# Performance work log

Measured on AMD Instinct MI355X. Metric: run time of the kernel, lower is better.

Reference implementation:

```python
import jax, jax.numpy as jnp
import numpy as np

N_INTERVALS = 40          # control intervals (240 = 6 * n)
DT = 0.25                 # interval_duration
CAR_WIDTH = 2.0
N_OBST = 3                # (13 - 4) / 3
BATCH = 131072


def _dynamics(state, u, t):
    # state: (..., 4) = [px, py, theta, v]; u: (..., 2) = [accel, omega]
    px, py, th, v = state[..., 0], state[..., 1], state[..., 2], state[..., 3]
    a, w = u[..., 0], u[..., 1]
    return jnp.stack([px + v * jnp.cos(th) * t,
                      py + v * jnp.sin(th) * t,
                      th + w * t,
                      v + a * t], axis=-1)


def setup_inputs() -> dict:
    key = jax.random.key(0)
    k1, k2, k3 = jax.random.split(key, 3)
    predictions = jax.random.normal(k1, (BATCH, 240), dtype=jnp.float32)
    targets = jax.random.normal(k2, (BATCH, 240), dtype=jnp.float32)
    inputs = jax.random.normal(k3, (BATCH, 13), dtype=jnp.float32)
    return {"predictions": predictions, "targets": targets, "inputs": inputs}


def reference(predictions, targets, inputs):
    n, t = N_INTERVALS, DT
    B = predictions.shape[0]

    mse = jnp.mean((predictions - targets) ** 2)

    x = predictions[:, : 4 * n].reshape(B, n, 4)          # states per interval
    u = predictions[:, 4 * n: 6 * n].reshape(B, n, 2)     # controls per interval
    x0 = inputs[:, :4]                                    # (B, 4)
    obstacles = inputs[:, 4:].reshape(B, N_OBST, 3)       # (B, 3, 3) = [ox, oy, r]

    # dynamics_error accumulates the per-interval residuals, then a single norm
    prev = jnp.concatenate([x0[:, None, :], x[:, :-1, :]], axis=1)  # (B, n, 4)
    dyn_resid = jnp.sum(x - _dynamics(prev, u, t), axis=1)          # (B, 4)
    dyn_err = jnp.linalg.norm(dyn_resid, axis=-1)                   # (B,)

    # obstacle term: sum over obstacles and states of dist - (r + car_width)^2
    dx = x[:, None, :, 0] - obstacles[:, :, None, 0]                # (B, 3, n)
    dy = x[:, None, :, 1] - obstacles[:, :, None, 1]
    dist = jnp.sqrt(dx * dx + dy * dy)
    rad2 = (obstacles[:, :, 2] + CAR_WIDTH) ** 2                    # (B, 3)
    obst_err = jnp.sum(dist - rad2[:, :, None], axis=(1, 2))        # (B,)

    constraint = jnp.mean(dyn_err + obst_err)
    return mse + constraint
```

## Files before the change

### kernel.cpp

```cpp
#include <hip/hip_runtime.h>


#define NTHREADS 256
#define ROWS_PER_BLOCK 64

__global__ __launch_bounds__(NTHREADS, 1) void constraint_main_kernel(
    const float* __restrict__ pred,
    const float* __restrict__ targ,
    const float* __restrict__ inp,
    float* __restrict__ partial,
    int B)
{
    const float DT = 0.25f;
    const int tid  = threadIdx.x;
    const int sub  = tid & 3;
    const int rloc = tid >> 2;
    const int row  = blockIdx.x * ROWS_PER_BLOCK + rloc;

    __shared__ float sinp[ROWS_PER_BLOCK * 13];
    {
        const int base = blockIdx.x * ROWS_PER_BLOCK * 13;
        const int tot  = ROWS_PER_BLOCK * 13;
        const int avail = B * 13 - base;
        for (int idx = tid; idx < tot; idx += NTHREADS) {
            float v = 0.0f;
            if (idx < avail) v = inp[base + idx];
            sinp[idx] = v;
        }
    }
    __syncthreads();

    float mse = 0.0f, cons = 0.0f;

    if (row < B) {
        const float4* p4 = reinterpret_cast<const float4*>(pred + (size_t)row * 240);
        const float4* t4 = reinterpret_cast<const float4*>(targ + (size_t)row * 240);

        float4 p[15], t[15];
        #pragma unroll
        for (int i = 0; i < 10; ++i) p[i] = p4[sub + 4 * i];
        #pragma unroll
        for (int i = 0; i < 5; ++i)  p[10 + i] = p4[40 + sub + 4 * i];
        #pragma unroll
        for (int i = 0; i < 10; ++i) t[i] = t4[sub + 4 * i];
        #pragma unroll
        for (int i = 0; i < 5; ++i)  t[10 + i] = t4[40 + sub + 4 * i];

        const float* in = &sinp[rloc * 13];
        const float ox0 = in[4],  oy0 = in[5];
        const float ox1 = in[7],  oy1 = in[8];
        const float ox2 = in[10], oy2 = in[11];

        float cv = 0.0f, sv = 0.0f, sum_dist = 0.0f;
        float sum_a = 0.0f, sum_w = 0.0f;
        float xlx = 0.0f, xly = 0.0f, xlth = 0.0f, xlv = 0.0f;

        #pragma unroll
        for (int i = 0; i < 10; ++i) {
            const int k = sub + 4 * i;
            const float4 pv = p[i];
            const float4 tv = t[i];
            float d0 = pv.x - tv.x, d1 = pv.y - tv.y;
            float d2 = pv.z - tv.z, d3 = pv.w - tv.w;
            mse += d0 * d0 + d1 * d1 + d2 * d2 + d3 * d3;

            if (k != 39) {
                float s, c;
                __sincosf(pv.z, &s, &c);
                cv += pv.w * c;
                sv += pv.w * s;
            } else {
                xlx = pv.x; xly = pv.y; xlth = pv.z; xlv = pv.w;
            }

            float dx, dy;
            dx = pv.x - ox0; dy = pv.y - oy0; sum_dist += sqrtf(dx * dx + dy * dy);
            dx = pv.x - ox1; dy = pv.y - oy1; sum_dist += sqrtf(dx * dx + dy * dy);
            dx = pv.x - ox2; dy = pv.y - oy2; sum_dist += sqrtf(dx * dx + dy * dy);
        }

        #pragma unroll
        for (int i = 0; i < 5; ++i) {
            const float4 pv = p[10 + i];
            const float4 tv = t[10 + i];
            float d0 = pv.x - tv.x, d1 = pv.y - tv.y;
            float d2 = pv.z - tv.z, d3 = pv.w - tv.w;
            mse += d0 * d0 + d1 * d1 + d2 * d2 + d3 * d3;
            sum_a += pv.x + pv.z;
            sum_w += pv.y + pv.w;
        }

        #pragma unroll
        for (int m = 1; m < 4; m <<= 1) {
            cv       += __shfl_xor(cv, m);
            sv       += __shfl_xor(sv, m);
            sum_a    += __shfl_xor(sum_a, m);
            sum_w    += __shfl_xor(sum_w, m);
            sum_dist += __shfl_xor(sum_dist, m);
        }

        const int lane = tid & 63;
        const int src  = lane | 3;
        xlx  = __shfl(xlx,  src);
        xly  = __shfl(xly,  src);
        xlth = __shfl(xlth, src);
        xlv  = __shfl(xlv,  src);

        if (sub == 0) {
            const float x0px = in[0], x0py = in[1], x0th = in[2], x0v = in[3];
            const float r0 = in[6]  + 2.0f;
            const float r1 = in[9]  + 2.0f;
            const float r2 = in[12] + 2.0f;
            float s, c;
            __sincosf(x0th, &s, &c);
            cv += x0v * c;
            sv += x0v * s;

            float rr0 = xlx  - x0px - DT * cv;
            float rr1 = xly  - x0py - DT * sv;
            float rr2 = xlth - x0th - DT * sum_w;
            float rr3 = xlv  - x0v  - DT * sum_a;
            float dyn_err = sqrtf(rr0 * rr0 + rr1 * rr1 + rr2 * rr2 + rr3 * rr3);
            float rad2sum = r0 * r0 + r1 * r1 + r2 * r2;
            cons = dyn_err + sum_dist - 40.0f * rad2sum;
        }
    }

    #pragma unroll
    for (int off = 32; off > 0; off >>= 1) {
        mse  += __shfl_down(mse,  off);
        cons += __shfl_down(cons, off);
    }

    __shared__ float smse[NTHREADS / 64];
    __shared__ float scons[NTHREADS / 64];
    const int wid  = threadIdx.x >> 6;
    const int lane = threadIdx.x & 63;
    if (lane == 0) { smse[wid] = mse; scons[wid] = cons; }
    __syncthreads();
    if (threadIdx.x == 0) {
        float m = smse[0] + smse[1] + smse[2] + smse[3];
        float c = scons[0] + scons[1] + scons[2] + scons[3];
        partial[2 * blockIdx.x]     = m;
        partial[2 * blockIdx.x + 1] = c;
    }
}

__global__ __launch_bounds__(256) void finalize_kernel(
    const float* __restrict__ partial, float* __restrict__ out,
    int nblocks, int B)
{
    float m = 0.0f, c = 0.0f;
    for (int i = threadIdx.x; i < nblocks; i += 256) {
        m += partial[2 * i];
        c += partial[2 * i + 1];
    }
    #pragma unroll
    for (int off = 32; off > 0; off >>= 1) {
        m += __shfl_down(m, off);
        c += __shfl_down(c, off);
    }
    __shared__ float sm[4], sc[4];
    const int wid  = threadIdx.x >> 6;
    const int lane = threadIdx.x & 63;
    if (lane == 0) { sm[wid] = m; sc[wid] = c; }
    __syncthreads();
    if (threadIdx.x == 0) {
        float mm = sm[0] + sm[1] + sm[2] + sm[3];
        float cc = sc[0] + sc[1] + sc[2] + sc[3];
        float nb = (float)B;
        out[0] = mm / (nb * 240.0f) + cc / nb;
    }
}

extern "C" void kernel_launch(void* const* d_in, const int* in_sizes, int n_in,
                              void* d_out, int out_size, void* d_ws, size_t ws_size,
                              hipStream_t stream) {
    const float* pred = (const float*)d_in[0];
    const float* targ = (const float*)d_in[1];
    const float* inp  = (const float*)d_in[2];
    float* out = (float*)d_out;
    float* ws  = (float*)d_ws;

    const int B = in_sizes[0] / 240;
    const int grid = (B + ROWS_PER_BLOCK - 1) / ROWS_PER_BLOCK;

    constraint_main_kernel<<<grid, NTHREADS, 0, stream>>>(pred, targ, inp, ws, B);
    finalize_kernel<<<1, 256, 0, stream>>>(ws, out, grid, B);
}
```

Baseline: 268.5 us.

## Stage predictions through LDS via direct global-to-LDS loads with coalesced access

Measured after the change: 268.9 us. Within noise of the previous version (+0.2%).

```diff
diff --git a/kernel.cpp b/kernel.cpp
--- a/kernel.cpp
+++ b/kernel.cpp
@@ -1,10 +1,13 @@
 #include <hip/hip_runtime.h>
+#include <stdint.h>
 
 
 #define NTHREADS 256
 #define ROWS_PER_BLOCK 64
-
-__global__ __launch_bounds__(NTHREADS, 1) void constraint_main_kernel(
+#define F4_PER_BLOCK (ROWS_PER_BLOCK * 60)
+#define F4_PER_THREAD (F4_PER_BLOCK / NTHREADS)
+
+__global__ __launch_bounds__(NTHREADS, 2) void constraint_main_kernel(
     const float* __restrict__ pred,
     const float* __restrict__ targ,
     const float* __restrict__ inp,
@@ -12,117 +15,139 @@
     int B)
 {
     const float DT = 0.25f;
-    const int tid  = threadIdx.x;
-    const int sub  = tid & 3;
-    const int rloc = tid >> 2;
-    const int row  = blockIdx.x * ROWS_PER_BLOCK + rloc;
-
-    __shared__ float sinp[ROWS_PER_BLOCK * 13];
+    const int tid = threadIdx.x;
+
+    __shared__ float4 spred[F4_PER_BLOCK];
+    __shared__ float  sinp[ROWS_PER_BLOCK * 13];
+
+    const size_t nf4     = (size_t)B * 60;
+    const size_t blk_f4  = (size_t)blockIdx.x * F4_PER_BLOCK;
+    const float4* pred4  = reinterpret_cast<const float4*>(pred);
+    const float4* targ4  = reinterpret_cast<const float4*>(targ);
+
+    #pragma unroll
+    for (int i = 0; i < F4_PER_THREAD; ++i) {
+        const int f = i * NTHREADS + tid;
+        size_t g = blk_f4 + (size_t)f;
+        if (g >= nf4) g = nf4 - 1;
+        __builtin_amdgcn_global_load_lds(
+            (const __attribute__((address_space(1))) void*)(pred4 + g),
+            (__attribute__((address_space(3))) void*)(&spred[f]),
+            16, 0, 0);
+    }
+
+    float4 t[F4_PER_THREAD];
+    #pragma unroll
+    for (int i = 0; i < F4_PER_THREAD; ++i) {
+        const int f = i * NTHREADS + tid;
+        size_t g = blk_f4 + (size_t)f;
+        if (g >= nf4) g = nf4 - 1;
+        t[i] = targ4[g];
+    }
+
     {
-        const int base = blockIdx.x * ROWS_PER_BLOCK * 13;
-        const int tot  = ROWS_PER_BLOCK * 13;
-        const int avail = B * 13 - base;
-        for (int idx = tid; idx < tot; idx += NTHREADS) {
+        const size_t base = (size_t)blockIdx.x * (ROWS_PER_BLOCK * 13);
+        const size_t lim  = (size_t)B * 13;
+        for (int idx = tid; idx < ROWS_PER_BLOCK * 13; idx += NTHREADS) {
             float v = 0.0f;
-            if (idx < avail) v = inp[base + idx];
+            if (base + idx < lim) v = inp[base + idx];
             sinp[idx] = v;
         }
     }
+
+    asm volatile("s_waitcnt vmcnt(0)" ::: "memory");
+    __builtin_amdgcn_sched_barrier(0);
+
+    float mse = 0.0f;
+    #pragma unroll
+    for (int i = 0; i < F4_PER_THREAD; ++i) {
+        const int f = i * NTHREADS + tid;
+        const float4 pv = spred[f];
+        const float4 tv = t[i];
+        float d0 = pv.x - tv.x, d1 = pv.y - tv.y;
+        float d2 = pv.z - tv.z, d3 = pv.w - tv.w;
+        mse += d0 * d0 + d1 * d1 + d2 * d2 + d3 * d3;
+    }
+
     __syncthreads();
 
-    float mse = 0.0f, cons = 0.0f;
-
-    if (row < B) {
-        const float4* p4 = reinterpret_cast<const float4*>(pred + (size_t)row * 240);
-        const float4* t4 = reinterpret_cast<const float4*>(targ + (size_t)row * 240);
-
-        float4 p[15], t[15];
-        #pragma unroll
-        for (int i = 0; i < 10; ++i) p[i] = p4[sub + 4 * i];
-        #pragma unroll
-        for (int i = 0; i < 5; ++i)  p[10 + i] = p4[40 + sub + 4 * i];
-        #pragma unroll
-        for (int i = 0; i < 10; ++i) t[i] = t4[sub + 4 * i];
-        #pragma unroll
-        for (int i = 0; i < 5; ++i)  t[10 + i] = t4[40 + sub + 4 * i];
-
-        const float* in = &sinp[rloc * 13];
-        const float ox0 = in[4],  oy0 = in[5];
-        const float ox1 = in[7],  oy1 = in[8];
-        const float ox2 = in[10], oy2 = in[11];
-
-        float cv = 0.0f, sv = 0.0f, sum_dist = 0.0f;
-        float sum_a = 0.0f, sum_w = 0.0f;
-        float xlx = 0.0f, xly = 0.0f, xlth = 0.0f, xlv = 0.0f;
-
-        #pragma unroll
-        for (int i = 0; i < 10; ++i) {
-            const int k = sub + 4 * i;
-            const float4 pv = p[i];
-            const float4 tv = t[i];
-            float d0 = pv.x - tv.x, d1 = pv.y - tv.y;
-            float d2 = pv.z - tv.z, d3 = pv.w - tv.w;
-            mse += d0 * d0 + d1 * d1 + d2 * d2 + d3 * d3;
-
-            if (k != 39) {
+    float cons = 0.0f;
+    {
+        const int sub  = tid & 3;
+        const int rloc = tid >> 2;
+        const int row  = blockIdx.x * ROWS_PER_BLOCK + rloc;
+
+        if (row < B) {
+            const float*  in   = &sinp[rloc * 13];
+            const float4* prow = &spred[rloc * 60];
+
+            const float ox0 = in[4],  oy0 = in[5];
+            const float ox1 = in[7],  oy1 = in[8];
+            const float ox2 = in[10], oy2 = in[11];
+
+            float cv = 0.0f, sv = 0.0f, sum_dist = 0.0f;
+            float sum_a = 0.0f, sum_w = 0.0f;
+            float xlx = 0.0f, xly = 0.0f, xlth = 0.0f, xlv = 0.0f;
+
+            #pragma unroll
+            for (int i = 0; i < 10; ++i) {
+                const int k = sub + 4 * i;
+                const float4 pv = prow[k];
+                if (k != 39) {
+                    float s, c;
+                    __sincosf(pv.z, &s, &c);
+                    cv += pv.w * c;
+                    sv += pv.w * s;
+                } else {
+                    xlx = pv.x; xly = pv.y; xlth = pv.z; xlv = pv.w;
+                }
+                float dx, dy;
+                dx = pv.x - ox0; dy = pv.y - oy0; sum_dist += sqrtf(dx * dx + dy * dy);
+                dx = pv.x - ox1; dy = pv.y - oy1; sum_dist += sqrtf(dx * dx + dy * dy);
+                dx = pv.x - ox2; dy = pv.y - oy2; sum_dist += sqrtf(dx * dx + dy * dy);
+            }
+
+            #pragma unroll
+            for (int i = 0; i < 5; ++i) {
+                const float4 pv = prow[40 + sub + 4 * i];
+                sum_a += pv.x + pv.z;
+                sum_w += pv.y + pv.w;
+            }
+
+            #pragma unroll
+            for (int m = 1; m < 4; m <<= 1) {
+                cv       += __shfl_xor(cv, m);
+                sv       += __shfl_xor(sv, m);
+                sum_a    += __shfl_xor(sum_a, m);
+                sum_w    += __shfl_xor(sum_w, m);
+                sum_dist += __shfl_xor(sum_dist, m);
+            }
+
+            const int lane = tid & 63;
+            const int src  = lane | 3;
+            xlx  = __shfl(xlx,  src);
+            xly  = __shfl(xly,  src);
+            xlth = __shfl(xlth, src);
+            xlv  = __shfl(xlv,  src);
+
+            if (sub == 0) {
+                const float x0px = in[0], x0py = in[1], x0th = in[2], x0v = in[3];
+                const float r0 = in[6]  + 2.0f;
+                const float r1 = in[9]  + 2.0f;
+                const float r2 = in[12] + 2.0f;
                 float s, c;
-                __sincosf(pv.z, &s, &c);
-                cv += pv.w * c;
-                sv += pv.w * s;
-            } else {
-                xlx = pv.x; xly = pv.y; xlth = pv.z; xlv = pv.w;
-            }
-
-            float dx, dy;
-            dx = pv.x - ox0; dy = pv.y - oy0; sum_dist += sqrtf(dx * dx + dy * dy);
-            dx = pv.x - ox1; dy = pv.y - oy1; sum_dist += sqrtf(dx * dx + dy * dy);
-            dx = pv.x - ox2; dy = pv.y - oy2; sum_dist += sqrtf(dx * dx + dy * dy);
-        }
-
-        #pragma unroll
-        for (int i = 0; i < 5; ++i) {
-            const float4 pv = p[10 + i];
-            const float4 tv = t[10 + i];
-            float d0 = pv.x - tv.x, d1 = pv.y - tv.y;
-            float d2 = pv.z - tv.z, d3 = pv.w - tv.w;
-            mse += d0 * d0 + d1 * d1 + d2 * d2 + d3 * d3;
-            sum_a += pv.x + pv.z;
-            sum_w += pv.y + pv.w;
-        }
-
-        #pragma unroll
-        for (int m = 1; m < 4; m <<= 1) {
-            cv       += __shfl_xor(cv, m);
-            sv       += __shfl_xor(sv, m);
-            sum_a    += __shfl_xor(sum_a, m);
-            sum_w    += __shfl_xor(sum_w, m);
-            sum_dist += __shfl_xor(sum_dist, m);
-        }
-
-        const int lane = tid & 63;
-        const int src  = lane | 3;
-        xlx  = __shfl(xlx,  src);
-        xly  = __shfl(xly,  src);
-        xlth = __shfl(xlth, src);
-        xlv  = __shfl(xlv,  src);
-
-        if (sub == 0) {
-            const float x0px = in[0], x0py = in[1], x0th = in[2], x0v = in[3];
-            const float r0 = in[6]  + 2.0f;
-            const float r1 = in[9]  + 2.0f;
-            const float r2 = in[12] + 2.0f;
-            float s, c;
-            __sincosf(x0th, &s, &c);
-            cv += x0v * c;
-            sv += x0v * s;
-
-            float rr0 = xlx  - x0px - DT * cv;
-            float rr1 = xly  - x0py - DT * sv;
-            float rr2 = xlth - x0th - DT * sum_w;
-            float rr3 = xlv  - x0v  - DT * sum_a;
-            float dyn_err = sqrtf(rr0 * rr0 + rr1 * rr1 + rr2 * rr2 + rr3 * rr3);
-            float rad2sum = r0 * r0 + r1 * r1 + r2 * r2;
-            cons = dyn_err + sum_dist - 40.0f * rad2sum;
+                __sincosf(x0th, &s, &c);
+                cv += x0v * c;
+                sv += x0v * s;
+
+                float rr0 = xlx  - x0px - DT * cv;
+                float rr1 = xly  - x0py - DT * sv;
+                float rr2 = xlth - x0th - DT * sum_w;
+                float rr3 = xlv  - x0v  - DT * sum_a;
+                float dyn_err = sqrtf(rr0 * rr0 + rr1 * rr1 + rr2 * rr2 + rr3 * rr3);
+                float rad2sum = r0 * r0 + r1 * r1 + r2 * r2;
+                cons = dyn_err + sum_dist - 40.0f * rad2sum;
+            }
         }
     }
 
```
